# Performance work log

Hardware: AMD Instinct MI355X
Metric: run time of the kernel (lower is better)

## Reference

```python
import jax, jax.numpy as jnp
import numpy as np

HIDDEN = 256
B, L = 4, 4096


def setup_inputs() -> dict:
    key = jax.random.key(0)
    k_in, k_q, k_k, k_v, k_len = jax.random.split(key, 5)
    inputs = jax.random.normal(k_in, (B, L, HIDDEN), dtype=jnp.float32)
    # torch.rand -> uniform [0,1)
    W_query = jax.random.uniform(k_q, (HIDDEN, HIDDEN), dtype=jnp.float32)
    W_key = jax.random.uniform(k_k, (HIDDEN, HIDDEN), dtype=jnp.float32)
    W_value = jax.random.uniform(k_v, (HIDDEN, HIDDEN), dtype=jnp.float32)
    lengths = jax.random.randint(k_len, (B,), 1, L + 1, dtype=jnp.int64)
    return {"inputs": inputs, "W_query": W_query, "W_key": W_key,
            "W_value": W_value, "lengths": lengths}


def reference(inputs, W_query, W_key, W_value, lengths):
    # lengths is unused by the original module (no masking applied).
    # QKV projections (batched matmul with shared weight)
    queries = jnp.einsum('blh,hd->bld', inputs, W_query)
    keys = jnp.einsum('blh,hd->bld', inputs, W_key)
    values = jnp.einsum('blh,hd->bld', inputs, W_value)
    # scaled dot-product attention, full [B, L, L] scores as in original
    scale = 1.0 / jnp.sqrt(jnp.asarray(HIDDEN, dtype=inputs.dtype))
    attn_scores = jnp.einsum('bqd,bkd->bqk', queries, keys) * scale
    attentions = jax.nn.softmax(attn_scores, axis=-1)
    weighted = jnp.einsum('bqk,bkd->bqd', attentions, values)
    return weighted
```

## Files before the change

kernel.cpp:

```cpp
#include <hip/hip_runtime.h>


typedef __bf16 bf16x8 __attribute__((ext_vector_type(8)));
typedef _Float16 f16x8 __attribute__((ext_vector_type(8)));
typedef _Float16 f16x4 __attribute__((ext_vector_type(4)));
typedef float floatx4 __attribute__((ext_vector_type(4)));

#define MFMA16B(a, b, c) __builtin_amdgcn_mfma_f32_16x16x32_bf16(a, b, c, 0, 0, 0)
#define MFMA16F(a, b, c) __builtin_amdgcn_mfma_f32_16x16x32_f16(a, b, c, 0, 0, 0)
#define GLOAD_LDS16(g, l)                                                  \
  __builtin_amdgcn_global_load_lds(                                        \
      (const __attribute__((address_space(1))) void *)(g),                 \
      (__attribute__((address_space(3))) void *)(l), 16, 0, 0)

#define HID 256
#define LSEQ 4096
#define NB 4
#define NTOK (NB * LSEQ)
#define PLANE ((size_t)NTOK * HID)
#define QSCALE 0.09016844005556021f


__device__ __forceinline__ void split_bf16(float v, __bf16 &h, __bf16 &l) {
  h = (__bf16)v;
  l = (__bf16)(v - (float)h);
}

template <int N>
__device__ __forceinline__ float dpp_ror(float v) {
  return __builtin_bit_cast(float,
      __builtin_amdgcn_update_dpp(0, __builtin_bit_cast(int, v),
                                  0x120 + N, 0xf, 0xf, true));
}
__device__ __forceinline__ float row_sum16(float v) {
  v += dpp_ror<1>(v);
  v += dpp_ror<2>(v);
  v += dpp_ror<4>(v);
  v += dpp_ror<8>(v);
  return v;
}
__device__ __forceinline__ float row_max16(float v) {
  v = fmaxf(v, dpp_ror<1>(v));
  v = fmaxf(v, dpp_ror<2>(v));
  v = fmaxf(v, dpp_ror<4>(v));
  v = fmaxf(v, dpp_ror<8>(v));
  return v;
}

__global__ __launch_bounds__(256) void wsplit(const float *__restrict__ Wq,
                                              const float *__restrict__ Wk,
                                              const float *__restrict__ Wv,
                                              __bf16 *__restrict__ Wht,
                                              __bf16 *__restrict__ Wlt) {
  __shared__ float tile[32][256];
  const int wsel = blockIdx.x;
  const int hb = blockIdx.y;
  const float *W = (wsel == 0) ? Wq : (wsel == 1) ? Wk : Wv;
  __bf16 *oh = Wht + wsel * HID * HID;
  __bf16 *ol = Wlt + wsel * HID * HID;
  const int t = threadIdx.x;
  #pragma unroll
  for (int p = 0; p < 8; ++p) {
    int r = p * 4 + (t >> 6);
    int c = (t & 63) * 4;
    *(floatx4 *)&tile[r][c] = *(const floatx4 *)&W[(hb * 32 + r) * HID + c];
  }
  __syncthreads();
  #pragma unroll
  for (int q = 0; q < 4; ++q) {
    int n = q * 64 + (t >> 2);
    int hs = (t & 3) * 8;
    bf16x8 hh, ll;
    #pragma unroll
    for (int i = 0; i < 8; ++i) {
      float v = tile[hs + i][n];
      __bf16 h, l;
      split_bf16(v, h, l);
      hh[i] = h; ll[i] = l;
    }
    *(bf16x8 *)&oh[n * HID + hb * 32 + hs] = hh;
    *(bf16x8 *)&ol[n * HID + hb * 32 + hs] = ll;
  }
}

__global__ __launch_bounds__(256, 2) void qkv_proj(const float *__restrict__ X,
                                                   const __bf16 *__restrict__ Wht,
                                                   const __bf16 *__restrict__ Wlt,
                                                   _Float16 *__restrict__ Qf,
                                                   _Float16 *__restrict__ Kf,
                                                   _Float16 *__restrict__ Vf) {
  __shared__ __bf16 WhS[64 * 256];
  __shared__ __bf16 WlS[64 * 256];
  _Float16 *Tf = (_Float16 *)WhS;

  const int mtile = blockIdx.x;
  const int col0 = blockIdx.y * 64;
  const int tid = threadIdx.x;
  const int w4 = tid >> 6;
  const int lane = tid & 63;
  const int quad = lane >> 4;
  const int ln = lane & 15;
  const int arow = mtile * 64 + w4 * 16 + ln;

  bf16x8 ah[8], al[8];
  #pragma unroll
  for (int kc = 0; kc < 8; ++kc) {
    const float *xp = X + (size_t)arow * HID + kc * 32 + quad * 8;
    floatx4 x0 = *(const floatx4 *)xp;
    floatx4 x1 = *(const floatx4 *)(xp + 4);
    #pragma unroll
    for (int j = 0; j < 4; ++j) {
      __bf16 h, l;
      split_bf16(x0[j], h, l); ah[kc][j] = h; al[kc][j] = l;
      split_bf16(x1[j], h, l); ah[kc][4 + j] = h; al[kc][4 + j] = l;
    }
  }

  const int srow = tid >> 2;
  const int sseg = tid & 3;

  bf16x8 pwh[8], pwl[8];
  {
    const size_t wbase = (size_t)(col0 + srow) * HID;
    #pragma unroll
    for (int j = 0; j < 8; ++j) {
      const int chunk = j * 4 + sseg;
      pwh[j] = *(const bf16x8 *)&Wht[wbase + chunk * 8];
      pwl[j] = *(const bf16x8 *)&Wlt[wbase + chunk * 8];
    }
  }

  for (int w = 0; w < 3; ++w) {
    __syncthreads();
    #pragma unroll
    for (int j = 0; j < 8; ++j) {
      const int chunk = j * 4 + sseg;
      const int dst = srow * 256 + ((chunk ^ (srow & 7)) << 3);
      *(bf16x8 *)&WhS[dst] = pwh[j];
      *(bf16x8 *)&WlS[dst] = pwl[j];
    }
    __syncthreads();

    if (w < 2) {
      const size_t wbase = (size_t)(w + 1) * HID * HID + (size_t)(col0 + srow) * HID;
      #pragma unroll
      for (int j = 0; j < 8; ++j) {
        const int chunk = j * 4 + sseg;
        pwh[j] = *(const bf16x8 *)&Wht[wbase + chunk * 8];
        pwl[j] = *(const bf16x8 *)&Wlt[wbase + chunk * 8];
      }
    }

    floatx4 acc[4] = {};
    #pragma unroll
    for (int kc = 0; kc < 8; ++kc) {
      #pragma unroll
      for (int nt = 0; nt < 4; ++nt) {
        const int a = (nt * 16 + ln) * 256 + (((kc * 4 + quad) ^ (ln & 7)) << 3);
        bf16x8 bh = *(const bf16x8 *)&WhS[a];
        bf16x8 bl = *(const bf16x8 *)&WlS[a];
        acc[nt] = MFMA16B(ah[kc], bh, acc[nt]);
        acc[nt] = MFMA16B(ah[kc], bl, acc[nt]);
        acc[nt] = MFMA16B(al[kc], bh, acc[nt]);
      }
    }

    if (w == 0) {
      #pragma unroll
      for (int nt = 0; nt < 4; ++nt) {
        #pragma unroll
        for (int r = 0; r < 4; ++r) {
          const int orow = mtile * 64 + w4 * 16 + quad * 4 + r;
          const int ocol = col0 + nt * 16 + ln;
          Qf[(size_t)orow * HID + ocol] = (_Float16)(acc[nt][r] * QSCALE);
        }
      }
    } else if (w == 1) {
      __syncthreads();
      #pragma unroll
      for (int nt = 0; nt < 4; ++nt) {
        #pragma unroll
        for (int r = 0; r < 4; ++r) {
          const int tok_l = w4 * 16 + quad * 4 + r;
          const int h_l = nt * 16 + ln;
          Tf[tok_l * 72 + h_l] = (_Float16)acc[nt][r];
        }
      }
      __syncthreads();
      #pragma unroll
      for (int i = 0; i < 2; ++i) {
        const int c = i * 256 + tid;
        const int lane_f = c & 63;
        const int ntf = (c >> 6) & 1;
        const int kcL = (c >> 7) & 1;
        const int t2 = (c >> 8) & 1;
        const int qf = lane_f >> 4;
        const int lnf = lane_f & 15;
        const int tok_l = t2 * 32 + ntf * 16 + lnf;
        f16x8 v = *(const f16x8 *)&Tf[tok_l * 72 + kcL * 32 + qf * 8];
        const int T = mtile * 2 + t2;
        const int kc = (col0 >> 5) + kcL;
        *(f16x8 *)&Kf[(size_t)T * 8192 + ((ntf * 8 + kc) * 64 + lane_f) * 8] = v;
      }
    } else {
      __syncthreads();
      #pragma unroll
      for (int nt = 0; nt < 4; ++nt) {
        #pragma unroll
        for (int r = 0; r < 4; ++r) {
          const int tok_l = w4 * 16 + quad * 4 + r;
          const int d_l = nt * 16 + ln;
          Tf[d_l * 72 + tok_l] = (_Float16)acc[nt][r];
        }
      }
      __syncthreads();
      #pragma unroll
      for (int i = 0; i < 2; ++i) {
        const int c = i * 256 + tid;
        const int lane_f = c & 63;
        const int dtL = (c >> 6) & 3;
        const int t2 = (c >> 8) & 1;
        const int qf = lane_f >> 4;
        const int lnf = lane_f & 15;
        const int d_l = dtL * 16 + lnf;
        f16x8 v = *(const f16x8 *)&Tf[d_l * 72 + t2 * 32 + qf * 8];
        const int T = mtile * 2 + t2;
        const int dt = (col0 >> 4) + dtL;
        *(f16x8 *)&Vf[(size_t)(T * 16 + dt) * 512 + lane_f * 8] = v;
      }
    }
  }
}

__global__ __launch_bounds__(256, 2) void attn(const _Float16 *__restrict__ Qf,
                                               const _Float16 *__restrict__ Kf,
                                               const _Float16 *__restrict__ Vf,
                                               _Float16 *__restrict__ Op,
                                               float *__restrict__ Mp,
                                               float *__restrict__ Lp) {
  __shared__ _Float16 KS0[8192];
  __shared__ _Float16 KS1[8192];
  __shared__ _Float16 PsS[4 * 16 * 72];

  const int bx = blockIdx.x;
  const int ks = bx & 1;
  const int qt = bx >> 1;
  const int b = qt >> 6;
  const int qtl = qt & 63;
  const int tid = threadIdx.x;
  const int w4 = tid >> 6;
  const int lane = tid & 63;
  const int quad = lane >> 4;
  const int ln = lane & 15;
  const int T0 = b * 128 + ks * 64;

  const int qtok = b * LSEQ + qtl * 64 + w4 * 16 + ln;
  f16x8 q[8];
  #pragma unroll
  for (int kc = 0; kc < 8; ++kc)
    q[kc] = *(const f16x8 *)&Qf[(size_t)qtok * HID + kc * 32 + quad * 8];

  const _Float16 *kuni = Kf + (size_t)T0 * 8192;
  const _Float16 *vuni = Vf + (size_t)T0 * 8192;
  const int koff = tid * 8;
  const int voff = lane * 8;

  #pragma unroll
  for (int i = 0; i < 4; ++i)
    GLOAD_LDS16(kuni + i * 2048 + koff, &KS0[i * 2048 + koff]);

  float m[4] = {-1e30f, -1e30f, -1e30f, -1e30f};
  float l[4] = {0.f, 0.f, 0.f, 0.f};
  floatx4 o[16] = {};

  for (int jm = 0; jm < 32; ++jm) {
    floatx4 s[4];
    __syncthreads();
    {
      const _Float16 *src = kuni + (size_t)(2 * jm + 1) * 8192 + koff;
      #pragma unroll
      for (int i = 0; i < 4; ++i)
        GLOAD_LDS16(src + i * 2048, &KS1[i * 2048 + koff]);
    }
    {
      floatx4 pa[2] = {}, pb[2] = {};
      #pragma unroll
      for (int nt = 0; nt < 2; ++nt)
        #pragma unroll
        for (int kc = 0; kc < 4; ++kc) {
          pa[nt] = MFMA16F(q[kc], *(const f16x8 *)(KS0 + (nt * 8 + kc) * 512 + voff), pa[nt]);
          pb[nt] = MFMA16F(q[4 + kc], *(const f16x8 *)(KS0 + (nt * 8 + 4 + kc) * 512 + voff), pb[nt]);
        }
      s[0] = pa[0] + pb[0];
      s[1] = pa[1] + pb[1];
    }
    __syncthreads();
    if (jm < 31) {
      const _Float16 *src = kuni + (size_t)(2 * jm + 2) * 8192 + koff;
      #pragma unroll
      for (int i = 0; i < 4; ++i)
        GLOAD_LDS16(src + i * 2048, &KS0[i * 2048 + koff]);
    }
    const _Float16 *va = vuni + (size_t)(2 * jm) * 8192;
    const _Float16 *vbp = vuni + (size_t)(2 * jm + 1) * 8192;
    f16x8 vb0[8];
    #pragma unroll
    for (int dt = 0; dt < 8; ++dt)
      vb0[dt] = *(const f16x8 *)(va + dt * 512 + voff);
    {
      floatx4 pa[2] = {}, pb[2] = {};
      #pragma unroll
      for (int nt = 0; nt < 2; ++nt)
        #pragma unroll
        for (int kc = 0; kc < 4; ++kc) {
          pa[nt] = MFMA16F(q[kc], *(const f16x8 *)(KS1 + (nt * 8 + kc) * 512 + voff), pa[nt]);
          pb[nt] = MFMA16F(q[4 + kc], *(const f16x8 *)(KS1 + (nt * 8 + 4 + kc) * 512 + voff), pb[nt]);
        }
      s[2] = pa[0] + pb[0];
      s[3] = pa[1] + pb[1];
    }
    f16x8 vb1[8];
    #pragma unroll
    for (int dt = 0; dt < 8; ++dt)
      vb1[dt] = *(const f16x8 *)(va + (8 + dt) * 512 + voff);

    float alpha[4];
    #pragma unroll
    for (int r = 0; r < 4; ++r) {
      const float tmax = row_max16(
          fmaxf(fmaxf(s[0][r], s[1][r]), fmaxf(s[2][r], s[3][r])));
      const float mn = fmaxf(m[r], tmax);
      const float al = exp2f(m[r] - mn);
      const float p0 = exp2f(s[0][r] - mn);
      const float p1 = exp2f(s[1][r] - mn);
      const float p2 = exp2f(s[2][r] - mn);
      const float p3 = exp2f(s[3][r] - mn);
      s[0][r] = p0; s[1][r] = p1; s[2][r] = p2; s[3][r] = p3;
      const float rs = row_sum16((p0 + p1) + (p2 + p3));
      l[r] = l[r] * al + rs;
      m[r] = mn;
      alpha[r] = al;
    }

    _Float16 *ps = PsS + w4 * 16 * 72;
    #pragma unroll
    for (int nt = 0; nt < 4; ++nt)
      #pragma unroll
      for (int r = 0; r < 4; ++r)
        ps[(quad * 4 + r) * 72 + nt * 16 + ln] = (_Float16)s[nt][r];

    const float amin = fminf(fminf(alpha[0], alpha[1]), fminf(alpha[2], alpha[3]));
    if (__any(amin < 1.0f)) {
      #pragma unroll
      for (int dt = 0; dt < 16; ++dt) {
        o[dt][0] *= alpha[0]; o[dt][1] *= alpha[1];
        o[dt][2] *= alpha[2]; o[dt][3] *= alpha[3];
      }
    }

    const f16x8 paA = *(const f16x8 *)&ps[ln * 72 + quad * 8];
    const f16x8 paB = *(const f16x8 *)&ps[ln * 72 + 32 + quad * 8];

    #pragma unroll
    for (int dt = 0; dt < 8; ++dt) o[dt] = MFMA16F(paA, vb0[dt], o[dt]);
    f16x8 vb2[8];
    #pragma unroll
    for (int dt = 0; dt < 8; ++dt)
      vb2[dt] = *(const f16x8 *)(vbp + dt * 512 + voff);
    #pragma unroll
    for (int dt = 0; dt < 8; ++dt) o[8 + dt] = MFMA16F(paA, vb1[dt], o[8 + dt]);
    f16x8 vb3[8];
    #pragma unroll
    for (int dt = 0; dt < 8; ++dt)
      vb3[dt] = *(const f16x8 *)(vbp + (8 + dt) * 512 + voff);
    #pragma unroll
    for (int dt = 0; dt < 8; ++dt) o[dt] = MFMA16F(paB, vb2[dt], o[dt]);
    #pragma unroll
    for (int dt = 0; dt < 8; ++dt) o[8 + dt] = MFMA16F(paB, vb3[dt], o[8 + dt]);
  }

  const int rowbase = b * LSEQ + qtl * 64 + w4 * 16 + quad * 4;
  #pragma unroll
  for (int dt = 0; dt < 16; ++dt)
    #pragma unroll
    for (int r = 0; r < 4; ++r)
      Op[(size_t)ks * PLANE + (size_t)(rowbase + r) * HID + dt * 16 + ln] =
          (_Float16)o[dt][r];
  if (ln == 0) {
    #pragma unroll
    for (int r = 0; r < 4; ++r) {
      Mp[ks * NTOK + rowbase + r] = m[r];
      Lp[ks * NTOK + rowbase + r] = l[r];
    }
  }
}

__global__ __launch_bounds__(256) void merge(const _Float16 *__restrict__ Op,
                                             const float *__restrict__ Mp,
                                             const float *__restrict__ Lp,
                                             float *__restrict__ Out) {
  const int row = blockIdx.x * 4 + (threadIdx.x >> 6);
  const int c = (threadIdx.x & 63) * 4;
  const float m0 = Mp[row], m1 = Mp[NTOK + row];
  const float l0 = Lp[row], l1 = Lp[NTOK + row];
  const float M = fmaxf(m0, m1);
  const float e0 = exp2f(m0 - M), e1 = exp2f(m1 - M);
  const float invL = 1.0f / (l0 * e0 + l1 * e1);
  const float w0 = e0 * invL, w1 = e1 * invL;
  f16x4 a = *(const f16x4 *)&Op[(size_t)row * HID + c];
  f16x4 b4 = *(const f16x4 *)&Op[PLANE + (size_t)row * HID + c];
  floatx4 out;
  #pragma unroll
  for (int i = 0; i < 4; ++i) out[i] = w0 * (float)a[i] + w1 * (float)b4[i];
  *(floatx4 *)&Out[(size_t)row * HID + c] = out;
}

extern "C" void kernel_launch(void *const *d_in, const int *in_sizes, int n_in,
                              void *d_out, int out_size, void *d_ws, size_t ws_size,
                              hipStream_t stream) {
  const float *X = (const float *)d_in[0];
  const float *Wq = (const float *)d_in[1];
  const float *Wk = (const float *)d_in[2];
  const float *Wv = (const float *)d_in[3];

  _Float16 *ws = (_Float16 *)d_ws;
  _Float16 *Qf = ws;
  _Float16 *Kf = Qf + PLANE;
  _Float16 *Vf = Kf + PLANE;
  __bf16 *Wht = (__bf16 *)(Vf + PLANE);
  __bf16 *Wlt = Wht + 3 * HID * HID;
  _Float16 *Op = (_Float16 *)(Wlt + 3 * HID * HID);
  float *Mp = (float *)(Op + 2 * PLANE);
  float *Lp = Mp + 2 * NTOK;

  wsplit<<<dim3(3, 8), 256, 0, stream>>>(Wq, Wk, Wv, Wht, Wlt);
  qkv_proj<<<dim3(256, 4), 256, 0, stream>>>(X, Wht, Wlt, Qf, Kf, Vf);
  attn<<<512, 256, 0, stream>>>(Qf, Kf, Vf, Op, Mp, Lp);
  merge<<<NTOK / 4, 256, 0, stream>>>(Op, Mp, Lp, (float *)d_out);
}
```

Measured before the change: 235.5 us.

## Split attention KV range three ways and halve qkv_proj LDS footprint

The attention kernel's key/value range is now split into three uneven chunks instead of two, launching 768 blocks rather than 512, and the merge kernel combines three partial outputs. The goal is better wave balance across CUs, helped by a launch bound of three blocks per CU. The projection kernel now stages the hi and lo weight halves one after another in a single LDS buffer with a separate transpose buffer, cutting shared memory so three blocks fit per CU. In exchange there are more barriers, and the extra partial plane adds merge traffic and workspace.

Result: slower. 378.2 us (+60.6%).

```diff
diff --git a/kernel.cpp b/kernel.cpp
--- a/kernel.cpp
+++ b/kernel.cpp
@@ -19,6 +19,7 @@
 #define NTOK (NB * LSEQ)
 #define PLANE ((size_t)NTOK * HID)
 #define QSCALE 0.09016844005556021f
+#define NKS 3
 
 
 __device__ __forceinline__ void split_bf16(float v, __bf16 &h, __bf16 &l) {
@@ -83,15 +84,14 @@
   }
 }
 
-__global__ __launch_bounds__(256, 2) void qkv_proj(const float *__restrict__ X,
+__global__ __launch_bounds__(256, 3) void qkv_proj(const float *__restrict__ X,
                                                    const __bf16 *__restrict__ Wht,
                                                    const __bf16 *__restrict__ Wlt,
                                                    _Float16 *__restrict__ Qf,
                                                    _Float16 *__restrict__ Kf,
                                                    _Float16 *__restrict__ Vf) {
-  __shared__ __bf16 WhS[64 * 256];
-  __shared__ __bf16 WlS[64 * 256];
-  _Float16 *Tf = (_Float16 *)WhS;
+  __shared__ __bf16 WS[64 * 256];
+  __shared__ _Float16 Tf[64 * 72];
 
   const int mtile = blockIdx.x;
   const int col0 = blockIdx.y * 64;
@@ -118,50 +118,58 @@
 
   const int srow = tid >> 2;
   const int sseg = tid & 3;
-
-  bf16x8 pwh[8], pwl[8];
-  {
-    const size_t wbase = (size_t)(col0 + srow) * HID;
+  const size_t wrowbase = (size_t)(col0 + srow) * HID;
+
+  bf16x8 pw[8];
+  #pragma unroll
+  for (int j = 0; j < 8; ++j)
+    pw[j] = *(const bf16x8 *)&Wht[wrowbase + (j * 4 + sseg) * 8];
+
+  for (int w = 0; w < 3; ++w) {
+    floatx4 acc[4] = {};
+    __syncthreads();
     #pragma unroll
     for (int j = 0; j < 8; ++j) {
       const int chunk = j * 4 + sseg;
-      pwh[j] = *(const bf16x8 *)&Wht[wbase + chunk * 8];
-      pwl[j] = *(const bf16x8 *)&Wlt[wbase + chunk * 8];
-    }
-  }
-
-  for (int w = 0; w < 3; ++w) {
+      *(bf16x8 *)&WS[srow * 256 + ((chunk ^ (srow & 7)) << 3)] = pw[j];
+    }
+    __syncthreads();
+    {
+      const size_t wbase = (size_t)w * HID * HID + wrowbase;
+      #pragma unroll
+      for (int j = 0; j < 8; ++j)
+        pw[j] = *(const bf16x8 *)&Wlt[wbase + (j * 4 + sseg) * 8];
+    }
+    #pragma unroll
+    for (int kc = 0; kc < 8; ++kc) {
+      #pragma unroll
+      for (int nt = 0; nt < 4; ++nt) {
+        const int a = (nt * 16 + ln) * 256 + (((kc * 4 + quad) ^ (ln & 7)) << 3);
+        bf16x8 bh = *(const bf16x8 *)&WS[a];
+        acc[nt] = MFMA16B(ah[kc], bh, acc[nt]);
+        acc[nt] = MFMA16B(al[kc], bh, acc[nt]);
+      }
+    }
     __syncthreads();
     #pragma unroll
     for (int j = 0; j < 8; ++j) {
       const int chunk = j * 4 + sseg;
-      const int dst = srow * 256 + ((chunk ^ (srow & 7)) << 3);
-      *(bf16x8 *)&WhS[dst] = pwh[j];
-      *(bf16x8 *)&WlS[dst] = pwl[j];
-    }
-    __syncthreads();
-
+      *(bf16x8 *)&WS[srow * 256 + ((chunk ^ (srow & 7)) << 3)] = pw[j];
+    }
+    __syncthreads();
     if (w < 2) {
-      const size_t wbase = (size_t)(w + 1) * HID * HID + (size_t)(col0 + srow) * HID;
-      #pragma unroll
-      for (int j = 0; j < 8; ++j) {
-        const int chunk = j * 4 + sseg;
-        pwh[j] = *(const bf16x8 *)&Wht[wbase + chunk * 8];
-        pwl[j] = *(const bf16x8 *)&Wlt[wbase + chunk * 8];
-      }
-    }
-
-    floatx4 acc[4] = {};
+      const size_t wbase = (size_t)(w + 1) * HID * HID + wrowbase;
+      #pragma unroll
+      for (int j = 0; j < 8; ++j)
+        pw[j] = *(const bf16x8 *)&Wht[wbase + (j * 4 + sseg) * 8];
+    }
     #pragma unroll
     for (int kc = 0; kc < 8; ++kc) {
       #pragma unroll
       for (int nt = 0; nt < 4; ++nt) {
         const int a = (nt * 16 + ln) * 256 + (((kc * 4 + quad) ^ (ln & 7)) << 3);
-        bf16x8 bh = *(const bf16x8 *)&WhS[a];
-        bf16x8 bl = *(const bf16x8 *)&WlS[a];
-        acc[nt] = MFMA16B(ah[kc], bh, acc[nt]);
+        bf16x8 bl = *(const bf16x8 *)&WS[a];
         acc[nt] = MFMA16B(ah[kc], bl, acc[nt]);
-        acc[nt] = MFMA16B(al[kc], bh, acc[nt]);
       }
     }
 
@@ -176,14 +184,12 @@
         }
       }
     } else if (w == 1) {
-      __syncthreads();
       #pragma unroll
       for (int nt = 0; nt < 4; ++nt) {
         #pragma unroll
         for (int r = 0; r < 4; ++r) {
           const int tok_l = w4 * 16 + quad * 4 + r;
-          const int h_l = nt * 16 + ln;
-          Tf[tok_l * 72 + h_l] = (_Float16)acc[nt][r];
+          Tf[tok_l * 72 + nt * 16 + ln] = (_Float16)acc[nt][r];
         }
       }
       __syncthreads();
@@ -203,14 +209,12 @@
         *(f16x8 *)&Kf[(size_t)T * 8192 + ((ntf * 8 + kc) * 64 + lane_f) * 8] = v;
       }
     } else {
-      __syncthreads();
       #pragma unroll
       for (int nt = 0; nt < 4; ++nt) {
         #pragma unroll
         for (int r = 0; r < 4; ++r) {
           const int tok_l = w4 * 16 + quad * 4 + r;
-          const int d_l = nt * 16 + ln;
-          Tf[d_l * 72 + tok_l] = (_Float16)acc[nt][r];
+          Tf[(nt * 16 + ln) * 72 + tok_l] = (_Float16)acc[nt][r];
         }
       }
       __syncthreads();
@@ -222,8 +226,7 @@
         const int t2 = (c >> 8) & 1;
         const int qf = lane_f >> 4;
         const int lnf = lane_f & 15;
-        const int d_l = dtL * 16 + lnf;
-        f16x8 v = *(const f16x8 *)&Tf[d_l * 72 + t2 * 32 + qf * 8];
+        f16x8 v = *(const f16x8 *)&Tf[(dtL * 16 + lnf) * 72 + t2 * 32 + qf * 8];
         const int T = mtile * 2 + t2;
         const int dt = (col0 >> 4) + dtL;
         *(f16x8 *)&Vf[(size_t)(T * 16 + dt) * 512 + lane_f * 8] = v;
@@ -232,7 +235,7 @@
   }
 }
 
-__global__ __launch_bounds__(256, 2) void attn(const _Float16 *__restrict__ Qf,
+__global__ __launch_bounds__(256, 3) void attn(const _Float16 *__restrict__ Qf,
                                                const _Float16 *__restrict__ Kf,
                                                const _Float16 *__restrict__ Vf,
                                                _Float16 *__restrict__ Op,
@@ -243,8 +246,8 @@
   __shared__ _Float16 PsS[4 * 16 * 72];
 
   const int bx = blockIdx.x;
-  const int ks = bx & 1;
-  const int qt = bx >> 1;
+  const int ks = bx % NKS;
+  const int qt = bx / NKS;
   const int b = qt >> 6;
   const int qtl = qt & 63;
   const int tid = threadIdx.x;
@@ -252,7 +255,10 @@
   const int lane = tid & 63;
   const int quad = lane >> 4;
   const int ln = lane & 15;
-  const int T0 = b * 128 + ks * 64;
+
+  const int MST[NKS + 1] = {0, 22, 43, 64};
+  const int ts = MST[ks];
+  const int nmac = MST[ks + 1] - ts;
 
   const int qtok = b * LSEQ + qtl * 64 + w4 * 16 + ln;
   f16x8 q[8];
@@ -260,8 +266,8 @@
   for (int kc = 0; kc < 8; ++kc)
     q[kc] = *(const f16x8 *)&Qf[(size_t)qtok * HID + kc * 32 + quad * 8];
 
-  const _Float16 *kuni = Kf + (size_t)T0 * 8192;
-  const _Float16 *vuni = Vf + (size_t)T0 * 8192;
+  const _Float16 *kuni = Kf + ((size_t)b * 128 + ts * 2) * 8192;
+  const _Float16 *vuni = Vf + ((size_t)b * 128 + ts * 2) * 8192;
   const int koff = tid * 8;
   const int voff = lane * 8;
 
@@ -273,7 +279,7 @@
   float l[4] = {0.f, 0.f, 0.f, 0.f};
   floatx4 o[16] = {};
 
-  for (int jm = 0; jm < 32; ++jm) {
+  for (int jm = 0; jm < nmac; ++jm) {
     floatx4 s[4];
     __syncthreads();
     {
@@ -295,7 +301,7 @@
       s[1] = pa[1] + pb[1];
     }
     __syncthreads();
-    if (jm < 31) {
+    if (jm < nmac - 1) {
       const _Float16 *src = kuni + (size_t)(2 * jm + 2) * 8192 + koff;
       #pragma unroll
       for (int i = 0; i < 4; ++i)
@@ -401,17 +407,25 @@
                                              float *__restrict__ Out) {
   const int row = blockIdx.x * 4 + (threadIdx.x >> 6);
   const int c = (threadIdx.x & 63) * 4;
-  const float m0 = Mp[row], m1 = Mp[NTOK + row];
-  const float l0 = Lp[row], l1 = Lp[NTOK + row];
-  const float M = fmaxf(m0, m1);
-  const float e0 = exp2f(m0 - M), e1 = exp2f(m1 - M);
-  const float invL = 1.0f / (l0 * e0 + l1 * e1);
-  const float w0 = e0 * invL, w1 = e1 * invL;
-  f16x4 a = *(const f16x4 *)&Op[(size_t)row * HID + c];
-  f16x4 b4 = *(const f16x4 *)&Op[PLANE + (size_t)row * HID + c];
-  floatx4 out;
-  #pragma unroll
-  for (int i = 0; i < 4; ++i) out[i] = w0 * (float)a[i] + w1 * (float)b4[i];
+  float M = -1e30f;
+  #pragma unroll
+  for (int i = 0; i < NKS; ++i) M = fmaxf(M, Mp[i * NTOK + row]);
+  float L = 0.f;
+  float e[NKS];
+  #pragma unroll
+  for (int i = 0; i < NKS; ++i) {
+    e[i] = exp2f(Mp[i * NTOK + row] - M);
+    L += Lp[i * NTOK + row] * e[i];
+  }
+  const float invL = 1.0f / L;
+  floatx4 out = {};
+  #pragma unroll
+  for (int i = 0; i < NKS; ++i) {
+    const float w = e[i] * invL;
+    f16x4 a = *(const f16x4 *)&Op[i * PLANE + (size_t)row * HID + c];
+    #pragma unroll
+    for (int j = 0; j < 4; ++j) out[j] += w * (float)a[j];
+  }
   *(floatx4 *)&Out[(size_t)row * HID + c] = out;
 }
 
@@ -430,11 +444,11 @@
   __bf16 *Wht = (__bf16 *)(Vf + PLANE);
   __bf16 *Wlt = Wht + 3 * HID * HID;
   _Float16 *Op = (_Float16 *)(Wlt + 3 * HID * HID);
-  float *Mp = (float *)(Op + 2 * PLANE);
-  float *Lp = Mp + 2 * NTOK;
+  float *Mp = (float *)(Op + (size_t)NKS * PLANE);
+  float *Lp = Mp + NKS * NTOK;
 
   wsplit<<<dim3(3, 8), 256, 0, stream>>>(Wq, Wk, Wv, Wht, Wlt);
   qkv_proj<<<dim3(256, 4), 256, 0, stream>>>(X, Wht, Wlt, Qf, Kf, Vf);
-  attn<<<512, 256, 0, stream>>>(Qf, Kf, Vf, Op, Mp, Lp);
+  attn<<<256 * NKS, 256, 0, stream>>>(Qf, Kf, Vf, Op, Mp, Lp);
   merge<<<NTOK / 4, 256, 0, stream>>>(Op, Mp, Lp, (float *)d_out);
 }
```
